# Kernel tuning notes

Hardware: AMD Instinct MI355X
Metric: run time of the kernel (lower is better)

The kernel has to match this reference:

```python
import jax, jax.numpy as jnp
import numpy as np

B, T, D = 8, 2048, 512
KQ, K = 32, 4  # DemandRouter defaults: k_query=32, k_topk=4


def setup_inputs() -> dict:
    key = jax.random.key(0)
    ks = jax.random.split(key, 9)

    def init(k, shape, fan_in):
        return (jax.random.normal(k, shape, jnp.float32) / np.sqrt(fan_in)).astype(jnp.float32)

    return dict(
        x=jax.random.normal(ks[0], (B, T, D), jnp.float32),
        # DemandRouter projections
        Wq=init(ks[1], (D, KQ), D), bq=jnp.zeros((KQ,), jnp.float32),
        Wk=init(ks[2], (D, KQ), D), bk=jnp.zeros((KQ,), jnp.float32),
        # System1 FFN (D -> 2D -> D) + LayerNorm
        W1=init(ks[3], (D, 2 * D), D), b1=jnp.zeros((2 * D,), jnp.float32),
        W2=init(ks[4], (2 * D, D), 2 * D), b2=jnp.zeros((D,), jnp.float32),
        ln_g=jnp.ones((D,), jnp.float32), ln_b=jnp.zeros((D,), jnp.float32),
        # System2 transform (2D -> 2D -> D)
        Wt1=init(ks[5], (2 * D, 2 * D), 2 * D), bt1=jnp.zeros((2 * D,), jnp.float32),
        Wt2=init(ks[6], (2 * D, D), 2 * D), bt2=jnp.zeros((D,), jnp.float32),
        # output projection
        Wo=init(ks[7], (D, D), D), bo=jnp.zeros((D,), jnp.float32),
    )


def reference(x, Wq, bq, Wk, bk, W1, b1, W2, b2, ln_g, ln_b, Wt1, bt1, Wt2, bt2, Wo, bo):
    # ---- DemandRouter: topk over query-key similarity, gather neighbors, mean ----
    q = x @ Wq + bq                      # [B,T,KQ]
    k = x @ Wk + bk                      # [B,T,KQ]
    sim = jnp.einsum('btk,bsk->bts', q, k) / np.float32(np.sqrt(KQ))  # [B,T,T]
    _, idx = jax.lax.top_k(sim, K)       # [B,T,K]
    # gather x[b, idx[b,t]] and mean over K neighbors -> [B,T,D]
    gathered = jax.vmap(lambda xb, ib: xb[ib])(x, idx).mean(axis=2)

    # ---- System1: residual FFN (exact GELU) + LayerNorm ----
    h = jax.nn.gelu(gathered @ W1 + b1, approximate=False) @ W2 + b2
    y = gathered + h
    mu = y.mean(-1, keepdims=True)
    var = y.var(-1, keepdims=True)
    y = (y - mu) / jnp.sqrt(var + 1e-5) * ln_g + ln_b  # [B,T,D]

    # ---- System2: sequential gated memory update over T ----
    def step(mem, xt):  # mem: [B,D], xt: [B,D]
        e = jnp.concatenate([xt, mem], axis=-1)                       # [B,2D]
        prop = jax.nn.gelu(e @ Wt1 + bt1, approximate=False) @ Wt2 + bt2  # [B,D]
        g = jax.nn.sigmoid(prop)
        mem = mem * (1.0 - g) + prop * g
        return mem, None

    mem0 = jnp.zeros((y.shape[0], y.shape[2]), y.dtype)
    mem_final, _ = jax.lax.scan(step, mem0, jnp.swapaxes(y, 0, 1))

    # pooled = system2_out[:, -1] == final memory
    return mem_final @ Wo + bo  # [B,D]
```

## Files before the change

kernel.cpp:

```cpp
#include <hip/hip_runtime.h>
#include <math.h>
#include <stdint.h>


using bf16x8 = __attribute__((ext_vector_type(8))) short;
using f32x4v = __attribute__((ext_vector_type(4))) float;
typedef unsigned long long ull;

__device__ inline unsigned short f2b(float f) {
  union { float f; unsigned int u; } v; v.f = f;
  unsigned int r = v.u + 0x7fffu + ((v.u >> 16) & 1u);
  return (unsigned short)(r >> 16);
}

__device__ inline float gelu_f(float x) {
  return 0.5f * x * (1.0f + erff(x * 0.70710678118654752f));
}

__device__ inline void ins4(float v, int i,
                            float& v0, int& i0, float& v1, int& i1,
                            float& v2, int& i2, float& v3, int& i3) {
  bool b0 = (v > v0) || (v == v0 && i < i0);
  bool b1 = (v > v1) || (v == v1 && i < i1);
  bool b2 = (v > v2) || (v == v2 && i < i2);
  bool b3 = (v > v3) || (v == v3 && i < i3);
  float nv3 = b2 ? v2 : (b3 ? v : v3); int ni3 = b2 ? i2 : (b3 ? i : i3);
  float nv2 = b1 ? v1 : (b2 ? v : v2); int ni2 = b1 ? i1 : (b2 ? i : i2);
  float nv1 = b0 ? v0 : (b1 ? v : v1); int ni1 = b0 ? i0 : (b1 ? i : i1);
  float nv0 = b0 ? v  : v0;            int ni0 = b0 ? i  : i0;
  v0=nv0; i0=ni0; v1=nv1; i1=ni1; v2=nv2; i2=ni2; v3=nv3; i3=ni3;
}


__global__ __launch_bounds__(256)
void wqk_kernel(const float* __restrict__ Wq, const float* __restrict__ Wk,
                float* __restrict__ wqk) {
  int id = blockIdx.x * 256 + threadIdx.x;
  int d = id >> 6, c = id & 63;
  wqk[id] = (c < 32) ? Wq[d * 32 + c] : Wk[d * 32 + (c - 32)];
}

__global__ __launch_bounds__(256)
void transpose_bf16_kernel(const float* __restrict__ src,
                           unsigned short* __restrict__ dst, int K, int N) {
  __shared__ float tile[32][33];
  int bk = blockIdx.x << 5, bn = blockIdx.y << 5;
  int c = threadIdx.x & 31, r8 = threadIdx.x >> 5;
  for (int r = r8; r < 32; r += 8) tile[r][c] = src[(size_t)(bk + r) * N + bn + c];
  __syncthreads();
  for (int r = r8; r < 32; r += 8) dst[(size_t)(bn + r) * K + bk + c] = f2b(tile[c][r]);
}


__global__ __launch_bounds__(256)
void qk_kernel(const float* __restrict__ x, const float* __restrict__ wqk,
               const float* __restrict__ bq, const float* __restrict__ bk,
               float* __restrict__ qkout) {
  __shared__ float xs[16][512];
  int tid = threadIdx.x;
  int b = blockIdx.x >> 7;
  int t0 = (blockIdx.x & 127) << 4;
  const float* xb = x + ((size_t)(b * 2048 + t0)) * 512;
#pragma unroll
  for (int i = 0; i < 8; ++i) {
    int f = i * 256 + tid;
    int r = f >> 7, c4 = f & 127;
    *(float4*)&xs[r][c4 * 4] = *(const float4*)&xb[(size_t)r * 512 + c4 * 4];
  }
  __syncthreads();
  int c = tid & 63, r4 = tid >> 6;
  float a0 = 0.f, a1 = 0.f, a2 = 0.f, a3 = 0.f;
#pragma unroll 4
  for (int d = 0; d < 512; ++d) {
    float w = wqk[d * 64 + c];
    a0 += xs[r4][d] * w;
    a1 += xs[r4 + 4][d] * w;
    a2 += xs[r4 + 8][d] * w;
    a3 += xs[r4 + 12][d] * w;
  }
  float bias = (c < 32) ? bq[c] : bk[c - 32];
  size_t base = ((size_t)(b * 2048 + t0)) * 64 + c;
  qkout[base + (size_t)r4 * 64] = a0 + bias;
  qkout[base + (size_t)(r4 + 4) * 64] = a1 + bias;
  qkout[base + (size_t)(r4 + 8) * 64] = a2 + bias;
  qkout[base + (size_t)(r4 + 12) * 64] = a3 + bias;
}

__global__ __launch_bounds__(256)
void topk_kernel(const float* __restrict__ qkb, int* __restrict__ idxout) {
  __shared__ float qs[16][36];
  __shared__ float ks[128][36];
  __shared__ float mv[16][16][4];
  __shared__ int   mi[16][16][4];
  int tid = threadIdx.x;
  int b = blockIdx.x >> 7;
  int t0 = (blockIdx.x & 127) << 4;
  const float* qb = qkb + ((size_t)b * 2048) * 64;
  if (tid < 128) {
    int r = tid >> 3, c4 = tid & 7;
    *(float4*)&qs[r][c4 * 4] = *(const float4*)&qb[(size_t)(t0 + r) * 64 + c4 * 4];
  }
  __syncthreads();
  int tl = tid >> 4, sl = tid & 15;
  float qv[32];
#pragma unroll
  for (int kk = 0; kk < 32; ++kk) qv[kk] = qs[tl][kk];
  float v0 = -INFINITY, v1 = -INFINITY, v2 = -INFINITY, v3 = -INFINITY;
  int i0 = 0x7fffffff, i1 = 0x7fffffff, i2 = 0x7fffffff, i3 = 0x7fffffff;
  for (int s0 = 0; s0 < 2048; s0 += 128) {
    __syncthreads();
#pragma unroll
    for (int p = 0; p < 4; ++p) {
      int f = p * 256 + tid;
      int r = f >> 3, c4 = f & 7;
      *(float4*)&ks[r][c4 * 4] =
          *(const float4*)&qb[(size_t)(s0 + r) * 64 + 32 + c4 * 4];
    }
    __syncthreads();
#pragma unroll
    for (int j = 0; j < 8; ++j) {
      int srow = j * 16 + sl;
      float accv = 0.f;
#pragma unroll
      for (int k4 = 0; k4 < 8; ++k4) {
        float4 kv = *(const float4*)&ks[srow][k4 * 4];
        accv += qv[k4 * 4 + 0] * kv.x + qv[k4 * 4 + 1] * kv.y +
                qv[k4 * 4 + 2] * kv.z + qv[k4 * 4 + 3] * kv.w;
      }
      ins4(accv, s0 + srow, v0, i0, v1, i1, v2, i2, v3, i3);
    }
  }
  mv[tl][sl][0] = v0; mv[tl][sl][1] = v1; mv[tl][sl][2] = v2; mv[tl][sl][3] = v3;
  mi[tl][sl][0] = i0; mi[tl][sl][1] = i1; mi[tl][sl][2] = i2; mi[tl][sl][3] = i3;
  __syncthreads();
  if (tid < 16) {
    float w0 = -INFINITY, w1 = -INFINITY, w2 = -INFINITY, w3 = -INFINITY;
    int a0 = 0x7fffffff, a1 = 0x7fffffff, a2 = 0x7fffffff, a3 = 0x7fffffff;
    for (int ss = 0; ss < 16; ++ss)
#pragma unroll
      for (int q = 0; q < 4; ++q)
        ins4(mv[tid][ss][q], mi[tid][ss][q], w0, a0, w1, a1, w2, a2, w3, a3);
    int4 o; o.x = a0; o.y = a1; o.z = a2; o.w = a3;
    *(int4*)&idxout[((size_t)(b * 2048 + t0 + tid)) * 4] = o;
  }
}

__global__ __launch_bounds__(128)
void gather_kernel(const float* __restrict__ x, const int* __restrict__ idx,
                   float* __restrict__ gf, unsigned short* __restrict__ gb) {
  int bt = blockIdx.x;
  int b = bt >> 11;
  const int4 iv = *(const int4*)&idx[(size_t)bt * 4];
  int tid = threadIdx.x;
  const float* xb = x + ((size_t)b * 2048) * 512;
  float4 p0 = *(const float4*)&xb[(size_t)iv.x * 512 + tid * 4];
  float4 p1 = *(const float4*)&xb[(size_t)iv.y * 512 + tid * 4];
  float4 p2 = *(const float4*)&xb[(size_t)iv.z * 512 + tid * 4];
  float4 p3 = *(const float4*)&xb[(size_t)iv.w * 512 + tid * 4];
  float4 m;
  m.x = (p0.x + p1.x + p2.x + p3.x) * 0.25f;
  m.y = (p0.y + p1.y + p2.y + p3.y) * 0.25f;
  m.z = (p0.z + p1.z + p2.z + p3.z) * 0.25f;
  m.w = (p0.w + p1.w + p2.w + p3.w) * 0.25f;
  *(float4*)&gf[(size_t)bt * 512 + tid * 4] = m;
  ushort4 u; u.x = f2b(m.x); u.y = f2b(m.y); u.z = f2b(m.z); u.w = f2b(m.w);
  *(ushort4*)&gb[(size_t)bt * 512 + tid * 4] = u;
}


template <int MODE>
__global__ __launch_bounds__(256, 2)
void gemm_bf16_k(const unsigned short* __restrict__ A,
                 const unsigned short* __restrict__ Bt,
                 const float* __restrict__ bias,
                 const float* __restrict__ resid,
                 void* __restrict__ outp, int M, int N, int K) {
  __shared__ unsigned short sA[128 * 32];
  __shared__ unsigned short sB[128 * 32];
  const int tid = threadIdx.x;
  const int lane = tid & 63, wave = tid >> 6;
  const int m0 = blockIdx.x * 128, n0 = blockIdx.y * 128;
  const int col16 = lane & 15, quad = lane >> 4;
  const int wm = wave >> 1, wn = wave & 1;
  f32x4v acc[4][4];
#pragma unroll
  for (int i = 0; i < 4; ++i)
#pragma unroll
    for (int j = 0; j < 4; ++j) {
      f32x4v z = {0.f, 0.f, 0.f, 0.f};
      acc[i][j] = z;
    }
  const int nkt = K >> 5;
  for (int kt = 0; kt < nkt; ++kt) {
    const int k0 = kt << 5;
#pragma unroll
    for (int p = 0; p < 2; ++p) {
      int f = p * 256 + tid;
      int row = f >> 2, q4 = f & 3;
      *(uint4*)&sA[row * 32 + q4 * 8] =
          *(const uint4*)(A + (size_t)(m0 + row) * K + k0 + q4 * 8);
      *(uint4*)&sB[row * 32 + q4 * 8] =
          *(const uint4*)(Bt + (size_t)(n0 + row) * K + k0 + q4 * 8);
    }
    __syncthreads();
    bf16x8 af[4], bfr[4];
#pragma unroll
    for (int i = 0; i < 4; ++i)
      af[i] = *(const bf16x8*)&sA[(wm * 64 + i * 16 + col16) * 32 + quad * 8];
#pragma unroll
    for (int j = 0; j < 4; ++j)
      bfr[j] = *(const bf16x8*)&sB[(wn * 64 + j * 16 + col16) * 32 + quad * 8];
#pragma unroll
    for (int i = 0; i < 4; ++i)
#pragma unroll
      for (int j = 0; j < 4; ++j)
        acc[i][j] = __builtin_amdgcn_mfma_f32_16x16x32_bf16(af[i], bfr[j],
                                                            acc[i][j], 0, 0, 0);
    __syncthreads();
  }
  float* outf = (float*)outp;
  unsigned short* outb = (unsigned short*)outp;
#pragma unroll
  for (int i = 0; i < 4; ++i)
#pragma unroll
    for (int j = 0; j < 4; ++j) {
      int col = n0 + wn * 64 + j * 16 + col16;
      float bs = bias[col];
#pragma unroll
      for (int r = 0; r < 4; ++r) {
        int row = m0 + wm * 64 + i * 16 + quad * 4 + r;
        float v = acc[i][j][r] + bs;
        if (MODE == 0) {
          outb[(size_t)row * N + col] = f2b(gelu_f(v));
        } else if (MODE == 1) {
          outf[(size_t)row * N + col] = v + resid[(size_t)row * N + col];
        } else {
          outf[(size_t)row * N + col] = v;
        }
      }
    }
}


__global__ __launch_bounds__(128)
void ln_kernel(const float* __restrict__ ypre, const float* __restrict__ lg,
               const float* __restrict__ lb, unsigned short* __restrict__ yb) {
  int row = blockIdx.x, tid = threadIdx.x;
  float4 v = *(const float4*)&ypre[(size_t)row * 512 + tid * 4];
  float s = v.x + v.y + v.z + v.w;
  float sq = v.x * v.x + v.y * v.y + v.z * v.z + v.w * v.w;
#pragma unroll
  for (int off = 1; off < 64; off <<= 1) {
    s += __shfl_xor(s, off, 64);
    sq += __shfl_xor(sq, off, 64);
  }
  __shared__ float red[4];
  if ((tid & 63) == 0) { red[(tid >> 6) * 2] = s; red[(tid >> 6) * 2 + 1] = sq; }
  __syncthreads();
  float S = red[0] + red[2], SQ = red[1] + red[3];
  float mu = S * (1.f / 512.f);
  float var = SQ * (1.f / 512.f) - mu * mu;
  float rstd = rsqrtf(var + 1e-5f);
  float4 g4 = *(const float4*)&lg[tid * 4];
  float4 b4 = *(const float4*)&lb[tid * 4];
  ushort4 u;
  u.x = f2b((v.x - mu) * rstd * g4.x + b4.x);
  u.y = f2b((v.y - mu) * rstd * g4.y + b4.y);
  u.z = f2b((v.z - mu) * rstd * g4.z + b4.z);
  u.w = f2b((v.w - mu) * rstd * g4.w + b4.w);
  *(ushort4*)&yb[(size_t)row * 512 + tid * 4] = u;
}


__global__ __launch_bounds__(256)
void system2_kernel(const float* __restrict__ Wt1, const float* __restrict__ Wt2,
                    const float* __restrict__ bt2, const float* __restrict__ xpart,
                    float* __restrict__ gubuf, float* __restrict__ membuf,
                    int* __restrict__ flagA, int* __restrict__ flagB,
                    float* __restrict__ memfinal) {
  __shared__ float WbT[32 * 516];
  __shared__ float Wt2S[1024 * 16];
  __shared__ float guS[1024];
  __shared__ float memS[512];
  __shared__ float parts1[256];
  __shared__ float red2[256];
  __shared__ float xbuf[16][32];

  const int t = threadIdx.x;
  const int team = blockIdx.x & 7;
  const int g = blockIdx.x >> 3;
  const int ucol0 = g << 5;
  const int mcol0 = g << 4;

  for (int idx = t; idx < 32 * 512; idx += 256) {
    int j = idx & 31, k = idx >> 5;
    WbT[j * 516 + k] = Wt1[(size_t)(512 + k) * 1024 + ucol0 + j];
  }
  for (int idx = t; idx < 1024 * 16; idx += 256) {
    int u = idx >> 4, dd = idx & 15;
    Wt2S[u * 16 + dd] = Wt2[(size_t)u * 512 + mcol0 + dd];
  }
  memS[t] = 0.f;
  memS[t + 256] = 0.f;
  const float bt2r = (t < 16) ? bt2[mcol0 + t] : 0.f;

  const int j = t & 31, c = t >> 5;
  const int w = t >> 4, dd = t & 15;
  const int lane = t & 63;
  const bool skipown = (t >> 3) == g;
  const float* xpTeam = xpart + (size_t)team * 2048 * 1024 + ucol0;
  const int ci = t >> 4, cp = (t & 15) << 1;
  float2 cur2 = *(const float2*)&xpTeam[(size_t)ci * 1024 + cp];
  __syncthreads();

  for (int s = 0; s < 2048; ++s) {
    const int par = s & 1;
    float* gub = gubuf + (size_t)(par * 8 + team) * 1024;
    float* memb = membuf + (size_t)(par * 8 + team) * 512;
    int* flA = flagA + (par * 8 + team) * 32;
    int* flB = flagB + (par * 8 + team) * 32;
    const int tagi = s + 1;

    if ((s & 15) == 0) {
      *(float2*)&xbuf[ci][cp] = cur2;
      int ns = s + 16 + ci; if (ns > 2047) ns = 2047;
      cur2 = *(const float2*)&xpTeam[(size_t)ns * 1024 + cp];
    }

    {
      const float* wrow = &WbT[j * 516 + c * 64];
      const float* mrow = &memS[c * 64];
      float p1 = 0.f;
#pragma unroll
      for (int i = 0; i < 64; i += 4) {
        float4 wv = *(const float4*)&wrow[i];
        float4 mv = *(const float4*)&mrow[i];
        p1 += wv.x * mv.x + wv.y * mv.y + wv.z * mv.z + wv.w * mv.w;
      }
      parts1[c * 32 + j] = p1;
    }
    __syncthreads();
    if (t < 32) {
      float u = xbuf[s & 15][t];
#pragma unroll
      for (int cc = 0; cc < 8; ++cc) u += parts1[cc * 32 + t];
      float gv = gelu_f(u);
      guS[ucol0 + t] = gv;
      __hip_atomic_store(&gub[ucol0 + t], gv, __ATOMIC_RELAXED,
                         __HIP_MEMORY_SCOPE_AGENT);
    }
    __syncthreads();
    if (t == 0)
      __hip_atomic_store(&flA[g], tagi, __ATOMIC_RELAXED,
                         __HIP_MEMORY_SCOPE_AGENT);
    {
      const bool need = (lane < 32) && (lane != g);
      const int* fp = &flA[lane & 31];
      while (true) {
        int f = need ? __hip_atomic_load(fp, __ATOMIC_RELAXED,
                                         __HIP_MEMORY_SCOPE_AGENT)
                     : tagi;
        if (__ballot(f == tagi) == ~0ull) break;
        __builtin_amdgcn_s_sleep(1);
      }
    }
    __builtin_amdgcn_fence(__ATOMIC_ACQUIRE, "workgroup");
    if (!skipown) {
      const ull* gu64 = (const ull*)gub;
      ull a = __hip_atomic_load(&gu64[2 * t], __ATOMIC_RELAXED,
                                __HIP_MEMORY_SCOPE_AGENT);
      ull b = __hip_atomic_load(&gu64[2 * t + 1], __ATOMIC_RELAXED,
                                __HIP_MEMORY_SCOPE_AGENT);
      guS[4 * t + 0] = __uint_as_float((unsigned)a);
      guS[4 * t + 1] = __uint_as_float((unsigned)(a >> 32));
      guS[4 * t + 2] = __uint_as_float((unsigned)b);
      guS[4 * t + 3] = __uint_as_float((unsigned)(b >> 32));
    }
    __syncthreads();

    {
      float p2 = 0.f;
#pragma unroll
      for (int i = 0; i < 64; ++i) {
        const int u = i * 16 + w;
        p2 += guS[u] * Wt2S[u * 16 + dd];
      }
      red2[w * 16 + dd] = p2;
    }
    __syncthreads();
    if (t < 16) {
      float prop = bt2r;
#pragma unroll
      for (int ww = 0; ww < 16; ++ww) prop += red2[ww * 16 + t];
      float gate = 1.f / (1.f + __expf(-prop));
      float mnew = memS[mcol0 + t] * (1.f - gate) + prop * gate;
      memS[mcol0 + t] = mnew;
      __hip_atomic_store(&memb[mcol0 + t], mnew, __ATOMIC_RELAXED,
                         __HIP_MEMORY_SCOPE_AGENT);
    }
    __syncthreads();
    if (t == 0)
      __hip_atomic_store(&flB[g], tagi, __ATOMIC_RELAXED,
                         __HIP_MEMORY_SCOPE_AGENT);
    {
      const bool need = (lane < 32) && (lane != g);
      const int* fp = &flB[lane & 31];
      while (true) {
        int f = need ? __hip_atomic_load(fp, __ATOMIC_RELAXED,
                                         __HIP_MEMORY_SCOPE_AGENT)
                     : tagi;
        if (__ballot(f == tagi) == ~0ull) break;
        __builtin_amdgcn_s_sleep(1);
      }
    }
    __builtin_amdgcn_fence(__ATOMIC_ACQUIRE, "workgroup");
    if (!skipown) {
      const ull* mem64 = (const ull*)memb;
      ull a = __hip_atomic_load(&mem64[t], __ATOMIC_RELAXED,
                                __HIP_MEMORY_SCOPE_AGENT);
      memS[2 * t + 0] = __uint_as_float((unsigned)a);
      memS[2 * t + 1] = __uint_as_float((unsigned)(a >> 32));
    }
    __syncthreads();
  }

  if (g == 0 && t < 128)
    *(float4*)&memfinal[(size_t)team * 512 + t * 4] = *(float4*)&memS[t * 4];
}


__global__ __launch_bounds__(256)
void out_gemv_kernel(const float* __restrict__ memf, const float* __restrict__ Wo,
                     const float* __restrict__ bo, float* __restrict__ out) {
  int gid = blockIdx.x * 256 + threadIdx.x;
  int b = gid >> 9, d = gid & 511;
  const float* mb = memf + (size_t)b * 512;
  float acc = bo[d];
#pragma unroll 8
  for (int k = 0; k < 512; ++k) acc += mb[k] * Wo[(size_t)k * 512 + d];
  out[gid] = acc;
}


extern "C" void kernel_launch(void* const* d_in, const int* in_sizes, int n_in,
                              void* d_out, int out_size, void* d_ws, size_t ws_size,
                              hipStream_t stream) {
  const float* x   = (const float*)d_in[0];
  const float* Wq  = (const float*)d_in[1];
  const float* bq  = (const float*)d_in[2];
  const float* Wk  = (const float*)d_in[3];
  const float* bk  = (const float*)d_in[4];
  const float* W1  = (const float*)d_in[5];
  const float* b1  = (const float*)d_in[6];
  const float* W2  = (const float*)d_in[7];
  const float* b2  = (const float*)d_in[8];
  const float* lng = (const float*)d_in[9];
  const float* lnb = (const float*)d_in[10];
  const float* Wt1 = (const float*)d_in[11];
  const float* bt1 = (const float*)d_in[12];
  const float* Wt2 = (const float*)d_in[13];
  const float* bt2 = (const float*)d_in[14];
  const float* Wo  = (const float*)d_in[15];
  const float* bo  = (const float*)d_in[16];
  float* out = (float*)d_out;

  char* ws = (char*)d_ws;
  size_t off = 0;
  auto alloc = [&](size_t bytes) -> void* {
    void* p = ws + off;
    off += (bytes + 255) & ~(size_t)255;
    return p;
  };
  float* qk             = (float*)alloc(8ull * 2048 * 64 * 4);
  int* idxb             = (int*)alloc(8ull * 2048 * 4 * 4);
  float* gathf          = (float*)alloc(16384ull * 512 * 4);
  unsigned short* gathb = (unsigned short*)alloc(16384ull * 512 * 2);
  unsigned short* h1b   = (unsigned short*)alloc(16384ull * 1024 * 2);
  float* ypre           = (float*)alloc(16384ull * 512 * 4);
  unsigned short* yb    = (unsigned short*)alloc(16384ull * 512 * 2);
  float* xpart          = (float*)alloc(16384ull * 1024 * 4);
  unsigned short* w1t   = (unsigned short*)alloc(1024ull * 512 * 2);
  unsigned short* w2t   = (unsigned short*)alloc(512ull * 1024 * 2);
  unsigned short* wt1t  = (unsigned short*)alloc(1024ull * 512 * 2);
  float* wqkb           = (float*)alloc(512ull * 64 * 4);
  float* gubuf          = (float*)alloc(2ull * 8 * 1024 * 4);
  float* membuf         = (float*)alloc(2ull * 8 * 512 * 4);
  int* flagA            = (int*)alloc(2ull * 8 * 32 * 4);
  int* flagB            = (int*)alloc(2ull * 8 * 32 * 4);
  float* memf           = (float*)alloc(8ull * 512 * 4);
  if (off > ws_size) return;

  wqk_kernel<<<128, 256, 0, stream>>>(Wq, Wk, wqkb);
  transpose_bf16_kernel<<<dim3(16, 32), 256, 0, stream>>>(W1, w1t, 512, 1024);
  transpose_bf16_kernel<<<dim3(32, 16), 256, 0, stream>>>(W2, w2t, 1024, 512);
  transpose_bf16_kernel<<<dim3(16, 32), 256, 0, stream>>>(Wt1, wt1t, 512, 1024);

  qk_kernel<<<1024, 256, 0, stream>>>(x, wqkb, bq, bk, qk);
  topk_kernel<<<1024, 256, 0, stream>>>(qk, idxb);
  gather_kernel<<<16384, 128, 0, stream>>>(x, idxb, gathf, gathb);

  gemm_bf16_k<0><<<dim3(128, 8), 256, 0, stream>>>(gathb, w1t, b1, nullptr, h1b,
                                                   16384, 1024, 512);
  gemm_bf16_k<1><<<dim3(128, 4), 256, 0, stream>>>(h1b, w2t, b2, gathf, ypre,
                                                   16384, 512, 1024);
  ln_kernel<<<16384, 128, 0, stream>>>(ypre, lng, lnb, yb);
  gemm_bf16_k<2><<<dim3(128, 8), 256, 0, stream>>>(yb, wt1t, bt1, nullptr, xpart,
                                                   16384, 1024, 512);

  system2_kernel<<<256, 256, 0, stream>>>(Wt1, Wt2, bt2, xpart, gubuf, membuf,
                                          flagA, flagB, memf);
  out_gemv_kernel<<<16, 256, 0, stream>>>(memf, Wo, bo, out);
}
```

Measured before the change: 8.807 ms.

## Restructure sequential scan: 64 blocks handle all batches, weights held in registers

The recurrent System2 scan moves from 8 independent teams of 32 blocks (one team per batch row) to a single team of 64 blocks that each process all 8 batch rows together. Each block now holds its slices of Wt1 and Wt2 in registers instead of shared memory, and computes small batched GEMVs (8 batch columns) with vector FMAs. The intent is to reuse each weight across the whole batch and to cut the number of blocks taking part in the per-step inter-block flag barrier. In exchange, each block does more work per step, must poll 64 flags instead of 32, adds extra __syncthreads, and exchanges larger global buffers every step.

```diff
diff --git a/kernel.cpp b/kernel.cpp
--- a/kernel.cpp
+++ b/kernel.cpp
@@ -5,6 +5,7 @@
 
 using bf16x8 = __attribute__((ext_vector_type(8))) short;
 using f32x4v = __attribute__((ext_vector_type(4))) float;
+using f4 = __attribute__((ext_vector_type(4))) float;
 typedef unsigned long long ull;
 
 __device__ inline unsigned short f2b(float f) {
@@ -272,90 +273,117 @@
 }
 
 
-__global__ __launch_bounds__(256)
+__global__ __launch_bounds__(256, 1)
 void system2_kernel(const float* __restrict__ Wt1, const float* __restrict__ Wt2,
                     const float* __restrict__ bt2, const float* __restrict__ xpart,
                     float* __restrict__ gubuf, float* __restrict__ membuf,
                     int* __restrict__ flagA, int* __restrict__ flagB,
                     float* __restrict__ memfinal) {
-  __shared__ float WbT[32 * 516];
-  __shared__ float Wt2S[1024 * 16];
-  __shared__ float guS[1024];
-  __shared__ float memS[512];
-  __shared__ float parts1[256];
-  __shared__ float red2[256];
-  __shared__ float xbuf[16][32];
+  __shared__ float memS[512 * 10];
+  __shared__ float guS[1024 * 10];
+  __shared__ float scratch[4096];
+  __shared__ float xbuf[16 * 8 * 16];
 
   const int t = threadIdx.x;
-  const int team = blockIdx.x & 7;
-  const int g = blockIdx.x >> 3;
-  const int ucol0 = g << 5;
-  const int mcol0 = g << 4;
-
-  for (int idx = t; idx < 32 * 512; idx += 256) {
-    int j = idx & 31, k = idx >> 5;
-    WbT[j * 516 + k] = Wt1[(size_t)(512 + k) * 1024 + ucol0 + j];
-  }
-  for (int idx = t; idx < 1024 * 16; idx += 256) {
-    int u = idx >> 4, dd = idx & 15;
-    Wt2S[u * 16 + dd] = Wt2[(size_t)u * 512 + mcol0 + dd];
-  }
-  memS[t] = 0.f;
-  memS[t + 256] = 0.f;
-  const float bt2r = (t < 16) ? bt2[mcol0 + t] : 0.f;
-
-  const int j = t & 31, c = t >> 5;
-  const int w = t >> 4, dd = t & 15;
+  const int g = blockIdx.x;
   const int lane = t & 63;
-  const bool skipown = (t >> 3) == g;
-  const float* xpTeam = xpart + (size_t)team * 2048 * 1024 + ucol0;
-  const int ci = t >> 4, cp = (t & 15) << 1;
-  float2 cur2 = *(const float2*)&xpTeam[(size_t)ci * 1024 + cp];
+
+  const int bq1 = t & 3, kc = (t >> 2) & 31, j2 = t >> 7;
+  const int bq2 = t & 3, uc = t >> 2;
+
+  f4 wA0[16], wA1[16];
+  {
+    const float* wsrc = Wt1 + (size_t)(512 + kc) * 1024 + g * 16 + j2 * 8;
+#pragma unroll
+    for (int kk = 0; kk < 16; ++kk) {
+      wA0[kk] = *(const f4*)(wsrc + (size_t)kk * 32 * 1024);
+      wA1[kk] = *(const f4*)(wsrc + (size_t)kk * 32 * 1024 + 4);
+    }
+  }
+  f4 wT0[16], wT1[16];
+  {
+    const float* wsrc = Wt2 + (size_t)uc * 512 + g * 8;
+#pragma unroll
+    for (int uu = 0; uu < 16; ++uu) {
+      wT0[uu] = *(const f4*)(wsrc + (size_t)uu * 64 * 512);
+      wT1[uu] = *(const f4*)(wsrc + (size_t)uu * 64 * 512 + 4);
+    }
+  }
+  const float bt2r = (t < 64) ? bt2[g * 8 + (t >> 3)] : 0.f;
+
+  for (int idx = t; idx < 512 * 10; idx += 256) memS[idx] = 0.f;
+
+  const float* xpB = xpart + (size_t)g * 16;
+  f4 cur0, cur1;
+  {
+    int f0 = t * 2, f1 = t * 2 + 1;
+    int si0 = f0 >> 5, b0 = (f0 >> 2) & 7, q0 = f0 & 3;
+    int si1 = f1 >> 5, b1 = (f1 >> 2) & 7, q1 = f1 & 3;
+    cur0 = *(const f4*)(xpB + (size_t)(b0 * 2048 + si0) * 1024 + q0 * 4);
+    cur1 = *(const f4*)(xpB + (size_t)(b1 * 2048 + si1) * 1024 + q1 * 4);
+  }
   __syncthreads();
 
   for (int s = 0; s < 2048; ++s) {
     const int par = s & 1;
-    float* gub = gubuf + (size_t)(par * 8 + team) * 1024;
-    float* memb = membuf + (size_t)(par * 8 + team) * 512;
-    int* flA = flagA + (par * 8 + team) * 32;
-    int* flB = flagB + (par * 8 + team) * 32;
+    float* gub = gubuf + (size_t)par * 8192;
+    float* memb = membuf + (size_t)par * 4096;
+    int* flA = flagA + par * 64;
+    int* flB = flagB + par * 64;
     const int tagi = s + 1;
 
     if ((s & 15) == 0) {
-      *(float2*)&xbuf[ci][cp] = cur2;
-      int ns = s + 16 + ci; if (ns > 2047) ns = 2047;
-      cur2 = *(const float2*)&xpTeam[(size_t)ns * 1024 + cp];
+      int f0 = t * 2, f1 = t * 2 + 1;
+      int si0 = f0 >> 5, b0 = (f0 >> 2) & 7, q0 = f0 & 3;
+      int si1 = f1 >> 5, b1 = (f1 >> 2) & 7, q1 = f1 & 3;
+      *(f4*)&xbuf[(si0 * 8 + b0) * 16 + q0 * 4] = cur0;
+      *(f4*)&xbuf[(si1 * 8 + b1) * 16 + q1 * 4] = cur1;
+      int r0 = s + 16 + si0; if (r0 > 2047) r0 = 2047;
+      int r1 = s + 16 + si1; if (r1 > 2047) r1 = 2047;
+      cur0 = *(const f4*)(xpB + (size_t)(b0 * 2048 + r0) * 1024 + q0 * 4);
+      cur1 = *(const f4*)(xpB + (size_t)(b1 * 2048 + r1) * 1024 + q1 * 4);
     }
 
     {
-      const float* wrow = &WbT[j * 516 + c * 64];
-      const float* mrow = &memS[c * 64];
-      float p1 = 0.f;
-#pragma unroll
-      for (int i = 0; i < 64; i += 4) {
-        float4 wv = *(const float4*)&wrow[i];
-        float4 mv = *(const float4*)&mrow[i];
-        p1 += wv.x * mv.x + wv.y * mv.y + wv.z * mv.z + wv.w * mv.w;
-      }
-      parts1[c * 32 + j] = p1;
-    }
-    __syncthreads();
-    if (t < 32) {
-      float u = xbuf[s & 15][t];
-#pragma unroll
-      for (int cc = 0; cc < 8; ++cc) u += parts1[cc * 32 + t];
+      f4 a0 = {0, 0, 0, 0}, a1 = a0, a2 = a0, a3 = a0;
+#pragma unroll
+      for (int kk = 0; kk < 16; ++kk) {
+        const int k = kk * 32 + kc;
+        float2 m2 = *(const float2*)&memS[k * 10 + bq1 * 2];
+        a0 += wA0[kk] * m2.x;
+        a1 += wA1[kk] * m2.x;
+        a2 += wA0[kk] * m2.y;
+        a3 += wA1[kk] * m2.y;
+      }
+      const int jb = j2 * 8, bb = bq1 * 2;
+#pragma unroll
+      for (int jj = 0; jj < 4; ++jj) {
+        scratch[((jb + jj) * 8 + bb) * 32 + kc] = a0[jj];
+        scratch[((jb + 4 + jj) * 8 + bb) * 32 + kc] = a1[jj];
+        scratch[((jb + jj) * 8 + bb + 1) * 32 + kc] = a2[jj];
+        scratch[((jb + 4 + jj) * 8 + bb + 1) * 32 + kc] = a3[jj];
+      }
+    }
+    __syncthreads();
+    if (t < 128) {
+      const int j = t >> 3, b = t & 7;
+      const float* pr = &scratch[(j * 8 + b) * 32];
+      f4 sv = *(const f4*)pr;
+#pragma unroll
+      for (int q = 1; q < 8; ++q) sv += *(const f4*)(pr + q * 4);
+      float u = sv.x + sv.y + sv.z + sv.w + xbuf[((s & 15) * 8 + b) * 16 + j];
       float gv = gelu_f(u);
-      guS[ucol0 + t] = gv;
-      __hip_atomic_store(&gub[ucol0 + t], gv, __ATOMIC_RELAXED,
+      guS[(g * 16 + j) * 10 + b] = gv;
+      __hip_atomic_store(&gub[(g * 16 + j) * 8 + b], gv, __ATOMIC_RELAXED,
                          __HIP_MEMORY_SCOPE_AGENT);
     }
     __syncthreads();
     if (t == 0)
       __hip_atomic_store(&flA[g], tagi, __ATOMIC_RELAXED,
                          __HIP_MEMORY_SCOPE_AGENT);
-    {
-      const bool need = (lane < 32) && (lane != g);
-      const int* fp = &flA[lane & 31];
+    if (t < 64) {
+      const bool need = (lane != g);
+      const int* fp = &flA[lane];
       while (true) {
         int f = need ? __hip_atomic_load(fp, __ATOMIC_RELAXED,
                                          __HIP_MEMORY_SCOPE_AGENT)
@@ -364,47 +392,66 @@
         __builtin_amdgcn_s_sleep(1);
       }
     }
+    __syncthreads();
     __builtin_amdgcn_fence(__ATOMIC_ACQUIRE, "workgroup");
-    if (!skipown) {
-      const ull* gu64 = (const ull*)gub;
-      ull a = __hip_atomic_load(&gu64[2 * t], __ATOMIC_RELAXED,
-                                __HIP_MEMORY_SCOPE_AGENT);
-      ull b = __hip_atomic_load(&gu64[2 * t + 1], __ATOMIC_RELAXED,
-                                __HIP_MEMORY_SCOPE_AGENT);
-      guS[4 * t + 0] = __uint_as_float((unsigned)a);
-      guS[4 * t + 1] = __uint_as_float((unsigned)(a >> 32));
-      guS[4 * t + 2] = __uint_as_float((unsigned)b);
-      guS[4 * t + 3] = __uint_as_float((unsigned)(b >> 32));
-    }
-    __syncthreads();
-
     {
-      float p2 = 0.f;
-#pragma unroll
-      for (int i = 0; i < 64; ++i) {
-        const int u = i * 16 + w;
-        p2 += guS[u] * Wt2S[u * 16 + dd];
-      }
-      red2[w * 16 + dd] = p2;
-    }
-    __syncthreads();
-    if (t < 16) {
-      float prop = bt2r;
-#pragma unroll
-      for (int ww = 0; ww < 16; ++ww) prop += red2[ww * 16 + t];
+      const ull* src = (const ull*)gub;
+      ull v[16];
+#pragma unroll
+      for (int i = 0; i < 16; ++i)
+        v[i] = __hip_atomic_load(&src[t * 16 + i], __ATOMIC_RELAXED,
+                                 __HIP_MEMORY_SCOPE_AGENT);
+#pragma unroll
+      for (int i = 0; i < 16; ++i) {
+        int w = t * 16 + i;
+        int u = (2 * w) >> 3, b = (2 * w) & 7;
+        *(ull*)&guS[u * 10 + b] = v[i];
+      }
+    }
+    __syncthreads();
+
+    {
+      f4 a0 = {0, 0, 0, 0}, a1 = a0, a2 = a0, a3 = a0;
+#pragma unroll
+      for (int uu = 0; uu < 16; ++uu) {
+        const int u = uu * 64 + uc;
+        float2 g2 = *(const float2*)&guS[u * 10 + bq2 * 2];
+        a0 += wT0[uu] * g2.x;
+        a1 += wT1[uu] * g2.x;
+        a2 += wT0[uu] * g2.y;
+        a3 += wT1[uu] * g2.y;
+      }
+      const int bb = bq2 * 2;
+#pragma unroll
+      for (int dj = 0; dj < 4; ++dj) {
+        scratch[(dj * 8 + bb) * 64 + uc] = a0[dj];
+        scratch[((dj + 4) * 8 + bb) * 64 + uc] = a1[dj];
+        scratch[(dj * 8 + bb + 1) * 64 + uc] = a2[dj];
+        scratch[((dj + 4) * 8 + bb + 1) * 64 + uc] = a3[dj];
+      }
+    }
+    __syncthreads();
+    if (t < 64) {
+      const int dd = t >> 3, b = t & 7;
+      const float* pr = &scratch[(dd * 8 + b) * 64];
+      f4 sv = *(const f4*)pr;
+#pragma unroll
+      for (int q = 1; q < 16; ++q) sv += *(const f4*)(pr + q * 4);
+      float prop = sv.x + sv.y + sv.z + sv.w + bt2r;
       float gate = 1.f / (1.f + __expf(-prop));
-      float mnew = memS[mcol0 + t] * (1.f - gate) + prop * gate;
-      memS[mcol0 + t] = mnew;
-      __hip_atomic_store(&memb[mcol0 + t], mnew, __ATOMIC_RELAXED,
+      const int mi = (g * 8 + dd) * 10 + b;
+      float mnew = memS[mi] * (1.f - gate) + prop * gate;
+      memS[mi] = mnew;
+      __hip_atomic_store(&memb[(g * 8 + dd) * 8 + b], mnew, __ATOMIC_RELAXED,
                          __HIP_MEMORY_SCOPE_AGENT);
     }
     __syncthreads();
     if (t == 0)
       __hip_atomic_store(&flB[g], tagi, __ATOMIC_RELAXED,
                          __HIP_MEMORY_SCOPE_AGENT);
-    {
-      const bool need = (lane < 32) && (lane != g);
-      const int* fp = &flB[lane & 31];
+    if (t < 64) {
+      const bool need = (lane != g);
+      const int* fp = &flB[lane];
       while (true) {
         int f = need ? __hip_atomic_load(fp, __ATOMIC_RELAXED,
                                          __HIP_MEMORY_SCOPE_AGENT)
@@ -413,19 +460,31 @@
         __builtin_amdgcn_s_sleep(1);
       }
     }
+    __syncthreads();
     __builtin_amdgcn_fence(__ATOMIC_ACQUIRE, "workgroup");
-    if (!skipown) {
-      const ull* mem64 = (const ull*)memb;
-      ull a = __hip_atomic_load(&mem64[t], __ATOMIC_RELAXED,
-                                __HIP_MEMORY_SCOPE_AGENT);
-      memS[2 * t + 0] = __uint_as_float((unsigned)a);
-      memS[2 * t + 1] = __uint_as_float((unsigned)(a >> 32));
-    }
-    __syncthreads();
-  }
-
-  if (g == 0 && t < 128)
-    *(float4*)&memfinal[(size_t)team * 512 + t * 4] = *(float4*)&memS[t * 4];
+    {
+      const ull* src = (const ull*)memb;
+      ull v[8];
+#pragma unroll
+      for (int i = 0; i < 8; ++i)
+        v[i] = __hip_atomic_load(&src[t * 8 + i], __ATOMIC_RELAXED,
+                                 __HIP_MEMORY_SCOPE_AGENT);
+#pragma unroll
+      for (int i = 0; i < 8; ++i) {
+        int w = t * 8 + i;
+        int k = (2 * w) >> 3, b = (2 * w) & 7;
+        *(ull*)&memS[k * 10 + b] = v[i];
+      }
+    }
+    __syncthreads();
+  }
+
+  if (g == 0) {
+    for (int idx = t; idx < 4096; idx += 256) {
+      int b = idx & 7, k = idx >> 3;
+      memfinal[(size_t)b * 512 + k] = memS[k * 10 + b];
+    }
+  }
 }
 
 
@@ -483,10 +542,10 @@
   unsigned short* w2t   = (unsigned short*)alloc(512ull * 1024 * 2);
   unsigned short* wt1t  = (unsigned short*)alloc(1024ull * 512 * 2);
   float* wqkb           = (float*)alloc(512ull * 64 * 4);
-  float* gubuf          = (float*)alloc(2ull * 8 * 1024 * 4);
-  float* membuf         = (float*)alloc(2ull * 8 * 512 * 4);
-  int* flagA            = (int*)alloc(2ull * 8 * 32 * 4);
-  int* flagB            = (int*)alloc(2ull * 8 * 32 * 4);
+  float* gubuf          = (float*)alloc(2ull * 8192 * 4);
+  float* membuf         = (float*)alloc(2ull * 4096 * 4);
+  int* flagA            = (int*)alloc(2ull * 64 * 4);
+  int* flagB            = (int*)alloc(2ull * 64 * 4);
   float* memf           = (float*)alloc(8ull * 512 * 4);
   if (off > ws_size) return;
 
@@ -507,7 +566,7 @@
   gemm_bf16_k<2><<<dim3(128, 8), 256, 0, stream>>>(yb, wt1t, bt1, nullptr, xpart,
                                                    16384, 1024, 512);
 
-  system2_kernel<<<256, 256, 0, stream>>>(Wt1, Wt2, bt2, xpart, gubuf, membuf,
-                                          flagA, flagB, memf);
+  system2_kernel<<<64, 256, 0, stream>>>(Wt1, Wt2, bt2, xpart, gubuf, membuf,
+                                         flagA, flagB, memf);
   out_gemv_kernel<<<16, 256, 0, stream>>>(memf, Wo, bo, out);
 }
```

New measurement: 22.76 ms. 158% more time.
